# Performance work log

Measured on AMD Instinct MI355X. Metric: run time of the kernel, lower is better.

Reference implementation:

```python
import jax, jax.numpy as jnp
import numpy as np

EPS = 1e-5

def _ln(x, g, b):
    m = jnp.mean(x, axis=-1, keepdims=True)
    v = jnp.mean((x - m) ** 2, axis=-1, keepdims=True)
    return (x - m) * jax.lax.rsqrt(v + EPS) * g + b

def setup_inputs() -> dict:
    key = jax.random.key(0)
    B, T, V, D = 32, 512, 16, 128
    ks = jax.random.split(key, 22)
    rn = lambda k, shp, sc: jax.random.normal(k, shp, jnp.float32) * sc
    inp = {
        "x": rn(ks[0], (B, T, V), 1.0),
        # per-variable GRN params (stacked over the V variables)
        "W1": rn(ks[1], (V, D), 1.0),          # fc1: Linear(1, D) weight per var
        "b1": rn(ks[2], (V, D), 0.02),
        "W2": rn(ks[3], (V, D, D), 1.0 / np.sqrt(D)),   # fc2: Linear(D, D)
        "b2": rn(ks[4], (V, D), 0.02),
        "Wg": rn(ks[5], (V, D, D), 1.0 / np.sqrt(D)),   # gate: Linear(D, D)
        "bg": rn(ks[6], (V, D), 0.02),
        "Ws": rn(ks[7], (V, D), 1.0),          # skip: Linear(1, D)
        "bs": rn(ks[8], (V, D), 0.02),
        "gamma": jnp.ones((V, D), jnp.float32),
        "beta": jnp.zeros((V, D), jnp.float32),
        # softmax GRN params: d_in = V*D, d_hidden = D, d_out = V
        "sW1": rn(ks[9], (D, V * D), 1.0 / np.sqrt(V * D)),
        "sb1": rn(ks[10], (D,), 0.02),
        "sW2": rn(ks[11], (V, D), 1.0 / np.sqrt(D)),
        "sb2": rn(ks[12], (V,), 0.02),
        "sWg": rn(ks[13], (V, D), 1.0 / np.sqrt(D)),
        "sbg": rn(ks[14], (V,), 0.02),
        "sWs": rn(ks[15], (V, V * D), 1.0 / np.sqrt(V * D)),
        "sbs": rn(ks[16], (V,), 0.02),
        "sgamma": jnp.ones((V,), jnp.float32),
        "sbeta": jnp.zeros((V,), jnp.float32),
    }
    return inp

def reference(x, W1, b1, W2, b2, Wg, bg, Ws, bs, gamma, beta,
              sW1, sb1, sW2, sb2, sWg, sbg, sWs, sbs, sgamma, sbeta):
    V, D = W1.shape
    lead = x.shape[:-1]
    xf = x.reshape(-1, V)                                  # (N, V)
    # ---- all per-variable GRNs batched over the var dim ----
    h = jax.nn.elu(xf[..., None] * W1 + b1)                # (N, V, D)
    h2 = jnp.einsum('nvd,vod->nvo', h, W2) + b2            # (N, V, D)
    g = jax.nn.sigmoid(jnp.einsum('nvd,vod->nvo', h, Wg) + bg)
    skip = xf[..., None] * Ws + bs                         # (N, V, D)
    stacked = _ln(g * h2 + (1.0 - g) * skip, gamma, beta)  # (N, V, D)
    # ---- softmax GRN over flattened embeddings ----
    flat = stacked.reshape(-1, V * D)                      # (N, V*D)
    hs = jax.nn.elu(flat @ sW1.T + sb1)                    # (N, D)
    h2s = hs @ sW2.T + sb2                                 # (N, V)
    gs = jax.nn.sigmoid(hs @ sWg.T + sbg)
    sks = flat @ sWs.T + sbs
    weights = jax.nn.softmax(_ln(gs * h2s + (1.0 - gs) * sks, sgamma, sbeta), axis=-1)
    processed = jnp.einsum('nvd,nv->nd', stacked, weights) # (N, D)
    return processed.reshape(*lead, D), weights.reshape(*lead, V)
```

## Files before the change

kernel.cpp:

```cpp
#include <hip/hip_runtime.h>
#include <hip/hip_bf16.h>
#include <math.h>

#define NVAR 16
#define ND 128
#define NVD 2048
#define NROWS 16384
#define RTA 256
#define NRB 32

typedef short s16x8 __attribute__((ext_vector_type(8)));
typedef short s16x4 __attribute__((ext_vector_type(4)));
typedef float f32x4 __attribute__((ext_vector_type(4)));
typedef unsigned short u16;

#define MFMA(a,b,c) __builtin_amdgcn_mfma_f32_16x16x32_bf16((a),(b),(c),0,0,0)

#define OFF_W2  0
#define OFF_WG  262144
#define OFF_SW1 524288
#define OFF_SWS 786432
#define OFF_SW2 819200
#define OFF_SWG 821248
#define WS_ELEMS 823296
#define OFF_STK 823296
#define STK_ELEMS ((size_t)NROWS*NVD)
#define WS_NEEDED_BYTES (((size_t)WS_ELEMS + STK_ELEMS)*2)
#define SV_ELEMS ((size_t)(NROWS/16)*2048)

__device__ __forceinline__ unsigned f2bf(float f){
    union { float f; unsigned u; } c; c.f = f;
    unsigned u = c.u;
    u += 0x7fffu + ((u >> 16) & 1u);
    return u >> 16;
}
__device__ __forceinline__ float bf2f(unsigned bits){
    union { unsigned u; float f; } c; c.u = bits << 16;
    return c.f;
}
__device__ __forceinline__ float eluf(float x){ return x > 0.f ? x : __expf(x) - 1.f; }
__device__ __forceinline__ float sigm(float x){
    return __builtin_amdgcn_rcpf(1.f + __expf(-x));
}

__device__ __forceinline__ int offHs(int r, int c){
    return r*128 + ((((c>>3) ^ (r&7))<<3) | (c&7));
}
__device__ __forceinline__ int offBig(int r, int c){
    return r*2048 + ((((c>>3) ^ (r&7))<<3) | (c&7));
}

__global__ void prep_kernel(const float* __restrict__ W2, const float* __restrict__ Wg,
                            const float* __restrict__ sW1, const float* __restrict__ sWs,
                            const float* __restrict__ sW2, const float* __restrict__ sWg,
                            u16* __restrict__ ws){
    int i = blockIdx.x*256 + threadIdx.x;
    if (i >= WS_ELEMS) return;
    float v;
    if      (i < OFF_WG)  v = W2[i];
    else if (i < OFF_SW1) v = Wg[i-OFF_WG];
    else if (i < OFF_SWS) v = sW1[i-OFF_SW1];
    else if (i < OFF_SW2) v = sWs[i-OFF_SWS];
    else if (i < OFF_SWG) v = sW2[i-OFF_SW2];
    else                  v = sWg[i-OFF_SWG];
    ws[i] = (u16)f2bf(v);
}

__global__ __launch_bounds__(512, 2)
void vsn_varA(const float* __restrict__ x,
              const float* __restrict__ W1, const float* __restrict__ b1,
              const float* __restrict__ b2, const float* __restrict__ bg,
              const float* __restrict__ Wsk, const float* __restrict__ bsk,
              const float* __restrict__ gamma, const float* __restrict__ beta,
              u16* __restrict__ ws)
{
    __shared__ u16 lw2[128*128];
    __shared__ u16 lwg[128*128];
    __shared__ float lp[8*128];
    __shared__ float lxv[RTA];

    const int t = threadIdx.x, w = t>>6, l = t&63;
    const int hr = l>>4, c16 = l&15;
    const int v = blockIdx.y;
    const int row0 = blockIdx.x*RTA;

    #pragma unroll
    for (int i=0;i<8;++i){
        int cid = i*512 + t;
        int mat = cid>>11, within = cid&2047;
        int r = within>>4, c8 = within&15;
        const u16* src = ws + (mat? OFF_WG:OFF_W2) + v*16384 + r*128 + c8*8;
        s16x8 val = *reinterpret_cast<const s16x8*>(src);
        u16* dst = (mat? lwg:lw2) + r*128 + ((c8 ^ (r&7))<<3);
        *reinterpret_cast<s16x8*>(dst) = val;
    }
    if (t < 128){
        lp[t]     = W1[v*ND+t];    lp[128+t] = b1[v*ND+t];
        lp[256+t] = b2[v*ND+t];    lp[384+t] = bg[v*ND+t];
        lp[512+t] = Wsk[v*ND+t];   lp[640+t] = bsk[v*ND+t];
        lp[768+t] = gamma[v*ND+t]; lp[896+t] = beta[v*ND+t];
    }
    if (t < RTA) lxv[t] = x[(size_t)(row0+t)*NVAR + v];
    __syncthreads();

    #pragma unroll 1
    for (int pass=0; pass<2; ++pass){
        const int lrow0 = (w + pass*8)*16;
        const float xv = lxv[lrow0 + c16];

        s16x8 B[4];
        #pragma unroll
        for (int ks=0;ks<4;++ks){
            s16x8 o;
            #pragma unroll
            for (int j=0;j<8;++j){
                int c = ks*32 + hr*8 + j;
                o[j] = (short)f2bf(eluf(xv*lp[c] + lp[128+c]));
            }
            B[ks] = o;
        }
        __builtin_amdgcn_sched_barrier(0);

        float y[8][4];
        #pragma unroll
        for (int ct=0; ct<8; ++ct){
            f32x4 a2 = {0.f,0.f,0.f,0.f}, ag = {0.f,0.f,0.f,0.f};
            const int wr = ct*16 + c16;
            #pragma unroll
            for (int ks=0;ks<4;++ks){
                int chunk = (ks*4 + hr) ^ (wr&7);
                s16x8 A2 = *reinterpret_cast<const s16x8*>(lw2 + wr*128 + chunk*8);
                a2 = MFMA(A2, B[ks], a2);
            }
            #pragma unroll
            for (int ks=0;ks<4;++ks){
                int chunk = (ks*4 + hr) ^ (wr&7);
                s16x8 Ag = *reinterpret_cast<const s16x8*>(lwg + wr*128 + chunk*8);
                ag = MFMA(Ag, B[ks], ag);
            }
            const int obb = ct*16 + hr*4;
            float4 b2v = *reinterpret_cast<const float4*>(&lp[256+obb]);
            float4 bgv = *reinterpret_cast<const float4*>(&lp[384+obb]);
            float4 wsv = *reinterpret_cast<const float4*>(&lp[512+obb]);
            float4 bsv = *reinterpret_cast<const float4*>(&lp[640+obb]);
            #pragma unroll
            for (int j=0;j<4;++j){
                float h2 = a2[j] + reinterpret_cast<const float*>(&b2v)[j];
                float gg = sigm(ag[j] + reinterpret_cast<const float*>(&bgv)[j]);
                float sk = xv*reinterpret_cast<const float*>(&wsv)[j]
                           + reinterpret_cast<const float*>(&bsv)[j];
                y[ct][j] = gg*h2 + (1.f-gg)*sk;
            }
            __builtin_amdgcn_sched_barrier(0);
        }
        float s = 0.f, q = 0.f;
        #pragma unroll
        for (int ct=0;ct<8;++ct)
            #pragma unroll
            for (int j=0;j<4;++j){ float yy = y[ct][j]; s += yy; q += yy*yy; }
        s += __shfl_xor(s, 16); s += __shfl_xor(s, 32);
        q += __shfl_xor(q, 16); q += __shfl_xor(q, 32);
        float mean = s*(1.f/ND);
        float inv  = rsqrtf(q*(1.f/ND) - mean*mean + 1e-5f);

        const int grp = blockIdx.x*16 + w + pass*8;
        u16* stkb = ws + OFF_STK + (size_t)v*SV_ELEMS + (size_t)grp*2048;
        #pragma unroll
        for (int ctp=0; ctp<4; ++ctp){
            s16x4 o0, o1;
            {
                int ct = ctp*2;
                const int obb = ct*16 + hr*4;
                float4 gm = *reinterpret_cast<const float4*>(&lp[768+obb]);
                float4 bt = *reinterpret_cast<const float4*>(&lp[896+obb]);
                #pragma unroll
                for (int j=0;j<4;++j){
                    float z = (y[ct][j]-mean)*inv*reinterpret_cast<const float*>(&gm)[j]
                              + reinterpret_cast<const float*>(&bt)[j];
                    o0[j] = (short)f2bf(z);
                }
            }
            {
                int ct = ctp*2 + 1;
                const int obb = ct*16 + hr*4;
                float4 gm = *reinterpret_cast<const float4*>(&lp[768+obb]);
                float4 bt = *reinterpret_cast<const float4*>(&lp[896+obb]);
                #pragma unroll
                for (int j=0;j<4;++j){
                    float z = (y[ct][j]-mean)*inv*reinterpret_cast<const float*>(&gm)[j]
                              + reinterpret_cast<const float*>(&bt)[j];
                    o1[j] = (short)f2bf(z);
                }
            }
            u16* bp = stkb + ctp*512 + c16*32;
            *reinterpret_cast<s16x4*>(bp + hr*4)      = o0;
            *reinterpret_cast<s16x4*>(bp + 16 + hr*4) = o1;
            __builtin_amdgcn_sched_barrier(0);
        }
    }
}

__device__ __forceinline__ s16x8 ldA(const u16* abuf, int vrel, int rg, int ctp, int n, int hr){
    int base = (((vrel*2 + rg)*4 + ctp)*16 + n)*32;
    int fn = (n>>1)&3;
    return *reinterpret_cast<const s16x8*>(abuf + base + ((hr ^ fn)<<3));
}

__global__ __launch_bounds__(256, 4)
void vsn_softB(const u16* __restrict__ ws,
               const float* __restrict__ sb1, const float* __restrict__ sb2,
               const float* __restrict__ sbg, const float* __restrict__ sbs,
               const float* __restrict__ sgamma, const float* __restrict__ sbeta,
               float* __restrict__ out_proc, float* __restrict__ out_w)
{
    __shared__ u16   abuf[8192];
    __shared__ u16   hsb[32*128];
    __shared__ float pps_[2*32*16];
    __shared__ float pph[32*16];
    __shared__ float ppg[32*16];
    __shared__ float sksf[32*16];
    __shared__ float wgtb[32*16];

    float* pps = pps_;

    const int t = threadIdx.x, w = t>>6, l = t&63;
    const int hr = l>>4, c16 = l&15;
    const int row0 = blockIdx.x * NRB;
    const int grp0 = row0 >> 4;
    const int col0 = w*32;
    const int rgs = w & 1;
    const int khf = w >> 1;

    const u16* stk  = ws + OFF_STK;
    const u16* sW1b = ws + OFF_SW1;
    const u16* sWsb = ws + OFF_SWS;

    f32x4 accHs00 = {0,0,0,0}, accHs01 = {0,0,0,0};
    f32x4 accHs10 = {0,0,0,0}, accHs11 = {0,0,0,0};
    f32x4 accSk = {0,0,0,0};

    #pragma unroll 1
    for (int kt=0; kt<8; ++kt){
        #pragma unroll
        for (int i=0;i<4;++i){
            int cid = i*256 + t;
            int vv  = kt*2 + (cid>>9);
            int n   = (cid>>2)&15;
            int u   = cid&3;
            const u16* src = stk + (size_t)vv*SV_ELEMS + (size_t)(grp0+((cid>>8)&1))*2048
                           + ((cid>>2)&63)*32 + u*8;
            s16x8 val = *reinterpret_cast<const s16x8*>(src);
            *reinterpret_cast<s16x8*>(abuf + (cid>>2)*32 + ((u ^ ((n>>1)&3))<<3)) = val;
        }
        __syncthreads();
        #pragma unroll
        for (int ks=0; ks<8; ++ks){
            const u16* bbase = sW1b + (size_t)(col0 + c16)*NVD + kt*256 + ks*32 + hr*8;
            s16x8 bf0 = *reinterpret_cast<const s16x8*>(bbase);
            s16x8 bf1 = *reinterpret_cast<const s16x8*>(bbase + (size_t)16*NVD);
            s16x8 af0 = ldA(abuf, ks>>2, 0, ks&3, c16, hr);
            s16x8 af1 = ldA(abuf, ks>>2, 1, ks&3, c16, hr);
            accHs00 = MFMA(af0, bf0, accHs00);
            accHs10 = MFMA(af1, bf0, accHs10);
            accHs01 = MFMA(af0, bf1, accHs01);
            accHs11 = MFMA(af1, bf1, accHs11);
        }
        #pragma unroll
        for (int kk=0; kk<4; ++kk){
            int ks = khf*4 + kk;
            s16x8 bf = *reinterpret_cast<const s16x8*>(
                sWsb + (size_t)c16*NVD + kt*256 + ks*32 + hr*8);
            s16x8 af = ldA(abuf, ks>>2, rgs, ks&3, c16, hr);
            accSk = MFMA(af, bf, accSk);
        }
        __syncthreads();
    }

    {
        float bb0 = sb1[col0 + c16];
        float bb1 = sb1[col0 + 16 + c16];
        #pragma unroll
        for (int j=0;j<4;++j){
            int r0 = hr*4 + j, r1 = 16 + hr*4 + j;
            hsb[offHs(r0, col0 + c16)]      = (u16)f2bf(eluf(accHs00[j] + bb0));
            hsb[offHs(r1, col0 + c16)]      = (u16)f2bf(eluf(accHs10[j] + bb0));
            hsb[offHs(r0, col0 + 16 + c16)] = (u16)f2bf(eluf(accHs01[j] + bb1));
            hsb[offHs(r1, col0 + 16 + c16)] = (u16)f2bf(eluf(accHs11[j] + bb1));
        }
        #pragma unroll
        for (int j=0;j<4;++j)
            pps[khf*512 + (rgs*16 + hr*4 + j)*16 + c16] = accSk[j];
    }
    __syncthreads();

    #pragma unroll
    for (int i=0;i<2;++i){
        int idx = i*256 + t;
        sksf[idx] = pps[idx] + pps[512+idx] + sbs[idx&15];
    }
    {
        const u16* Bsrc = (w < 2) ? (ws + OFF_SW2) : (ws + OFF_SWG);
        int rg = w & 1;
        f32x4 acc = {0,0,0,0};
        #pragma unroll
        for (int ks=0; ks<4; ++ks){
            int rr = rg*16 + c16;
            int chunk = (ks*4 + hr) ^ (rr&7);
            s16x8 af = *reinterpret_cast<const s16x8*>(hsb + rr*128 + chunk*8);
            s16x8 bf = *reinterpret_cast<const s16x8*>(Bsrc + c16*ND + ks*32 + hr*8);
            acc = MFMA(af, bf, acc);
        }
        float* dst = (w < 2) ? pph : ppg;
        #pragma unroll
        for (int j=0;j<4;++j)
            dst[(rg*16 + hr*4 + j)*16 + c16] = acc[j];
    }
    __syncthreads();

    #pragma unroll
    for (int it=0; it<2; ++it){
        int r = it*16 + (t>>4), vv = t & 15;
        float h2s = pph[r*16+vv] + sb2[vv];
        float gs  = sigm(ppg[r*16+vv] + sbg[vv]);
        float yv  = gs*h2s + (1.f-gs)*sksf[r*16+vv];
        float ssum = yv, qsum = yv*yv;
        #pragma unroll
        for (int m=1;m<16;m<<=1){ ssum += __shfl_xor(ssum,m,16); qsum += __shfl_xor(qsum,m,16); }
        float mean = ssum*(1.f/NVAR);
        float var  = qsum*(1.f/NVAR) - mean*mean;
        float z = (yv-mean)*rsqrtf(var+1e-5f)*sgamma[vv] + sbeta[vv];
        float mx = z;
        #pragma unroll
        for (int m=1;m<16;m<<=1) mx = fmaxf(mx, __shfl_xor(mx,m,16));
        float e = __expf(z-mx);
        float es = e;
        #pragma unroll
        for (int m=1;m<16;m<<=1) es += __shfl_xor(es,m,16);
        float wgt = e * __builtin_amdgcn_rcpf(es);
        wgtb[r*16+vv] = wgt;
        out_w[(size_t)(row0+r)*NVAR + vv] = wgt;
    }
    __syncthreads();

    #pragma unroll
    for (int it=0; it<2; ++it){
        int idx = it*256 + t;
        int r = idx>>4, cu = idx&15;
        int ctp = cu>>2, u = cu&3;
        int grp = (row0+r)>>4, n = r&15;
        float acc[8] = {0,0,0,0,0,0,0,0};
        #pragma unroll
        for (int v=0; v<NVAR; ++v){
            float wv = wgtb[r*16 + v];
            const u16* sp = stk + (size_t)v*SV_ELEMS + (size_t)grp*2048
                          + (ctp*16+n)*32 + u*8;
            s16x8 sv = *reinterpret_cast<const s16x8*>(sp);
            #pragma unroll
            for (int k=0;k<8;++k) acc[k] += bf2f((u16)sv[k]) * wv;
        }
        float* op = out_proc + (size_t)(row0+r)*ND + ctp*32 + u*8;
        float4 lo = { acc[0], acc[1], acc[2], acc[3] };
        float4 hi = { acc[4], acc[5], acc[6], acc[7] };
        *reinterpret_cast<float4*>(op)     = lo;
        *reinterpret_cast<float4*>(op + 4) = hi;
    }
}

__global__ __launch_bounds__(512, 4)
void vsn_fused(const float* __restrict__ x,
               const float* __restrict__ W1, const float* __restrict__ b1,
               const float* __restrict__ b2, const float* __restrict__ bg,
               const float* __restrict__ Wsk, const float* __restrict__ bsk,
               const float* __restrict__ gamma, const float* __restrict__ beta,
               const float* __restrict__ sb1, const float* __restrict__ sb2,
               const float* __restrict__ sbg, const float* __restrict__ sbs,
               const float* __restrict__ sgamma, const float* __restrict__ sbeta,
               const u16* __restrict__ ws,
               float* __restrict__ out_proc, float* __restrict__ out_w)
{
    __shared__ u16   big[16*2048];
    __shared__ u16   hsb[16*128];
    __shared__ float pp[8*256];
    __shared__ float psumbuf[256];
    __shared__ float sksbuf[256];
    __shared__ float sx[256];

    float* psum  = psumbuf;
    float* psum2 = psumbuf + 128;

    const int t   = threadIdx.x;
    const int w   = t >> 6;
    const int l   = t & 63;
    const int hr  = l >> 4;
    const int c16 = l & 15;
    const int row0 = blockIdx.x * 16;
    const int orow = w*16 + c16;

    if (t < 256) sx[t] = x[row0*NVAR + t];
    __syncthreads();

    const u16* W2b = ws + OFF_W2;
    const u16* Wgb = ws + OFF_WG;

    for (int v = 0; v < NVAR; ++v){
        #pragma unroll
        for (int i = 0; i < 4; ++i){
            int idx = i*512 + t;
            int r = idx >> 7, d = idx & 127;
            float hv = eluf(sx[r*NVAR+v]*W1[v*ND+d] + b1[v*ND+d]);
            big[offBig(r, v*ND+d)] = (u16)f2bf(hv);
        }
        __syncthreads();

        s16x8 A[4];
        #pragma unroll
        for (int ks = 0; ks < 4; ++ks)
            A[ks] = *reinterpret_cast<const s16x8*>(&big[offBig(c16, v*ND + ks*32 + hr*8)]);
        const s16x8* B2p = reinterpret_cast<const s16x8*>(W2b + v*ND*ND + orow*ND + hr*8);
        const s16x8* Bgp = reinterpret_cast<const s16x8*>(Wgb + v*ND*ND + orow*ND + hr*8);
        f32x4 acc2 = {0.f,0.f,0.f,0.f}, accg = {0.f,0.f,0.f,0.f};
        #pragma unroll
        for (int ks = 0; ks < 4; ++ks) acc2 = MFMA(A[ks], B2p[ks*4], acc2);
        #pragma unroll
        for (int ks = 0; ks < 4; ++ks) accg = MFMA(A[ks], Bgp[ks*4], accg);

        const float b2v = b2[v*ND+orow], bgv = bg[v*ND+orow];
        const float wsv = Wsk[v*ND+orow], bsv = bsk[v*ND+orow];
        float y[4];
        #pragma unroll
        for (int j = 0; j < 4; ++j){
            int r = hr*4 + j;
            float h2 = acc2[j] + b2v;
            float g  = sigm(accg[j] + bgv);
            float sk = sx[r*NVAR+v]*wsv + bsv;
            y[j] = g*h2 + (1.f-g)*sk;
        }
        float s[4], q[4];
        #pragma unroll
        for (int j=0;j<4;++j){ s[j]=y[j]; q[j]=y[j]*y[j]; }
        #pragma unroll
        for (int m=1; m<16; m<<=1){
            #pragma unroll
            for (int j=0;j<4;++j){
                s[j] += __shfl_xor(s[j], m, 16);
                q[j] += __shfl_xor(q[j], m, 16);
            }
        }
        if (c16 == 0){
            #pragma unroll
            for (int j=0;j<4;++j){
                psum [(hr*4+j)*8 + w] = s[j];
                psum2[(hr*4+j)*8 + w] = q[j];
            }
        }
        __syncthreads();

        if (t < 16){
            float ss=0.f, qq=0.f;
            #pragma unroll
            for (int ww=0; ww<8; ++ww){ ss += psum[t*8+ww]; qq += psum2[t*8+ww]; }
            float mean = ss*(1.f/ND);
            float var  = qq*(1.f/ND) - mean*mean;
            sksbuf[t]      = mean;
            sksbuf[16 + t] = rsqrtf(var + 1e-5f);
        }
        __syncthreads();

        const float gm = gamma[v*ND+orow], bt = beta[v*ND+orow];
        #pragma unroll
        for (int j=0;j<4;++j){
            int r = hr*4 + j;
            float z = (y[j]-sksbuf[r])*sksbuf[16+r]*gm + bt;
            big[offBig(r, v*ND+orow)] = (u16)f2bf(z);
        }
    }
    __syncthreads();

    const u16* sW1b = ws + OFF_SW1;
    {
        f32x4 acc0 = {0,0,0,0}, acc1 = {0,0,0,0};
        const s16x8* Bp = reinterpret_cast<const s16x8*>(sW1b + orow*NVD + hr*8);
        #pragma unroll 8
        for (int ks = 0; ks < 64; ks += 2){
            s16x8 A0 = *reinterpret_cast<const s16x8*>(&big[offBig(c16, ks*32 + hr*8)]);
            s16x8 A1 = *reinterpret_cast<const s16x8*>(&big[offBig(c16, (ks+1)*32 + hr*8)]);
            acc0 = MFMA(A0, Bp[ks*4],     acc0);
            acc1 = MFMA(A1, Bp[(ks+1)*4], acc1);
        }
        float bb = sb1[orow];
        #pragma unroll
        for (int j=0;j<4;++j){
            int r = hr*4 + j;
            hsb[offHs(r, orow)] = (u16)f2bf(eluf(acc0[j] + acc1[j] + bb));
        }
    }
    const u16* sWsb = ws + OFF_SWS;
    {
        f32x4 acc = {0,0,0,0};
        const s16x8* Bp = reinterpret_cast<const s16x8*>(sWsb + c16*NVD + hr*8);
        #pragma unroll
        for (int kk = 0; kk < 8; ++kk){
            int ks = w*8 + kk;
            s16x8 Af = *reinterpret_cast<const s16x8*>(&big[offBig(c16, ks*32 + hr*8)]);
            acc = MFMA(Af, Bp[ks*4], acc);
        }
        #pragma unroll
        for (int j=0;j<4;++j)
            pp[w*256 + (hr*4+j)*16 + c16] = acc[j];
    }
    __syncthreads();

    if (t < 256){
        float a = sbs[t & 15];
        #pragma unroll
        for (int ww=0; ww<8; ++ww) a += pp[ww*256 + t];
        sksbuf[t] = a;
    }
    __syncthreads();

    {
        const u16* Bsrc = (w < 4) ? (ws + OFF_SW2) : (ws + OFF_SWG);
        const int m = w & 3;
        s16x8 Af = *reinterpret_cast<const s16x8*>(&hsb[offHs(c16, m*32 + hr*8)]);
        s16x8 Bf = *reinterpret_cast<const s16x8*>(Bsrc + c16*ND + m*32 + hr*8);
        f32x4 z4 = {0,0,0,0};
        f32x4 acc = MFMA(Af, Bf, z4);
        #pragma unroll
        for (int j=0;j<4;++j)
            pp[w*256 + (hr*4+j)*16 + c16] = acc[j];
    }
    __syncthreads();

    if (t < 256){
        int r = t >> 4, vv = t & 15;
        float h2s = sb2[vv], gp = sbg[vv];
        #pragma unroll
        for (int j=0;j<4;++j){ h2s += pp[j*256 + t]; gp += pp[(4+j)*256 + t]; }
        float gs = sigm(gp);
        float yv = gs*h2s + (1.f-gs)*sksbuf[t];
        float ssum = yv, qsum = yv*yv;
        #pragma unroll
        for (int m=1;m<16;m<<=1){ ssum += __shfl_xor(ssum,m,16); qsum += __shfl_xor(qsum,m,16); }
        float mean = ssum*(1.f/NVAR);
        float var  = qsum*(1.f/NVAR) - mean*mean;
        float z = (yv-mean)*rsqrtf(var+1e-5f)*sgamma[vv] + sbeta[vv];
        float mx = z;
        #pragma unroll
        for (int m=1;m<16;m<<=1) mx = fmaxf(mx, __shfl_xor(mx,m,16));
        float e = __expf(z-mx);
        float es = e;
        #pragma unroll
        for (int m=1;m<16;m<<=1) es += __shfl_xor(es,m,16);
        float wgt = e/es;
        psumbuf[t] = wgt;
        out_w[(row0+r)*NVAR + vv] = wgt;
    }
    __syncthreads();

    if (t < 256){
        int r = t >> 4, d8 = (t & 15)*8;
        float acc[8] = {0,0,0,0,0,0,0,0};
        #pragma unroll
        for (int v=0; v<NVAR; ++v){
            float wv = psumbuf[r*NVAR + v];
            s16x8 sv = *reinterpret_cast<const s16x8*>(&big[offBig(r, v*ND + d8)]);
            #pragma unroll
            for (int k=0;k<8;++k) acc[k] += bf2f((u16)sv[k]) * wv;
        }
        float* op = &out_proc[(row0+r)*ND + d8];
        #pragma unroll
        for (int k=0;k<8;++k) op[k] = acc[k];
    }
}

extern "C" void kernel_launch(void* const* d_in, const int* in_sizes, int n_in,
                              void* d_out, int out_size, void* d_ws, size_t ws_size,
                              hipStream_t stream) {
    (void)in_sizes; (void)n_in; (void)out_size;
    const float* x     = (const float*)d_in[0];
    const float* W1    = (const float*)d_in[1];
    const float* b1    = (const float*)d_in[2];
    const float* W2    = (const float*)d_in[3];
    const float* b2    = (const float*)d_in[4];
    const float* Wg    = (const float*)d_in[5];
    const float* bg    = (const float*)d_in[6];
    const float* Wsk   = (const float*)d_in[7];
    const float* bsk   = (const float*)d_in[8];
    const float* gamma = (const float*)d_in[9];
    const float* beta  = (const float*)d_in[10];
    const float* sW1   = (const float*)d_in[11];
    const float* sb1   = (const float*)d_in[12];
    const float* sW2   = (const float*)d_in[13];
    const float* sb2   = (const float*)d_in[14];
    const float* sWg   = (const float*)d_in[15];
    const float* sbg   = (const float*)d_in[16];
    const float* sWs   = (const float*)d_in[17];
    const float* sbs   = (const float*)d_in[18];
    const float* sgam  = (const float*)d_in[19];
    const float* sbet  = (const float*)d_in[20];

    u16* ws = (u16*)d_ws;
    float* out_proc = (float*)d_out;
    float* out_w    = out_proc + (size_t)NROWS * ND;

    prep_kernel<<<(WS_ELEMS + 255)/256, 256, 0, stream>>>(W2, Wg, sW1, sWs, sW2, sWg, ws);

    if (ws_size >= WS_NEEDED_BYTES) {
        vsn_varA<<<dim3(NROWS/RTA, NVAR), 512, 0, stream>>>(
            x, W1, b1, b2, bg, Wsk, bsk, gamma, beta, ws);
        vsn_softB<<<NROWS/NRB, 256, 0, stream>>>(
            ws, sb1, sb2, sbg, sbs, sgam, sbet, out_proc, out_w);
    } else {
        vsn_fused<<<NROWS/16, 512, 0, stream>>>(
            x, W1, b1, b2, bg, Wsk, bsk, gamma, beta,
            sb1, sb2, sbg, sbs, sgam, sbet, ws, out_proc, out_w);
    }
}
```

Before: 113.1 us.

## Double-buffer stacked-activation tiles in softmax GRN kernel with register prefetch

Converts the K-loop of the softmax-GRN kernel to a double-buffered LDS scheme. The next tile's stacked activations are loaded into registers before the MFMA work on the current tile and written to the alternate buffer afterwards, so one barrier per iteration is removed and global latency is hidden behind compute. The cost is 16 KB more shared memory per block, which may reduce occupancy under launch_bounds(256,4), plus extra live registers for the prefetched tiles.

```diff
diff --git a/kernel.cpp b/kernel.cpp
--- a/kernel.cpp
+++ b/kernel.cpp
@@ -213,7 +213,7 @@
                const float* __restrict__ sgamma, const float* __restrict__ sbeta,
                float* __restrict__ out_proc, float* __restrict__ out_w)
 {
-    __shared__ u16   abuf[8192];
+    __shared__ u16   abuf[2*8192];
     __shared__ u16   hsb[32*128];
     __shared__ float pps_[2*32*16];
     __shared__ float pph[32*16];
@@ -235,31 +235,48 @@
     const u16* sW1b = ws + OFF_SW1;
     const u16* sWsb = ws + OFF_SWS;
 
+    const int c0 = t, c1 = 256+t, c2 = 512+t, c3 = 768+t;
+    #define SRCOFF(cid) ((size_t)(grp0+(((cid)>>8)&1))*2048 + (size_t)(((cid)>>2)&63)*32 + ((cid)&3)*8)
+    #define VREL(cid)   ((cid)>>9)
+    #define DSTOFF(cid) (((cid)>>2)*32 + ((((cid)&3) ^ ((((cid)>>3)&3)))<<3))
+    const size_t s0 = SRCOFF(c0), s1 = SRCOFF(c1), s2 = SRCOFF(c2), s3 = SRCOFF(c3);
+    const int    v0 = VREL(c0),   v1 = VREL(c1),   v2 = VREL(c2),   v3 = VREL(c3);
+    const int    d0 = DSTOFF(c0), d1 = DSTOFF(c1), d2 = DSTOFF(c2), d3 = DSTOFF(c3);
+
     f32x4 accHs00 = {0,0,0,0}, accHs01 = {0,0,0,0};
     f32x4 accHs10 = {0,0,0,0}, accHs11 = {0,0,0,0};
     f32x4 accSk = {0,0,0,0};
 
+    s16x8 t0 = *reinterpret_cast<const s16x8*>(stk + (size_t)(0+v0)*SV_ELEMS + s0);
+    s16x8 t1 = *reinterpret_cast<const s16x8*>(stk + (size_t)(0+v1)*SV_ELEMS + s1);
+    s16x8 t2 = *reinterpret_cast<const s16x8*>(stk + (size_t)(0+v2)*SV_ELEMS + s2);
+    s16x8 t3 = *reinterpret_cast<const s16x8*>(stk + (size_t)(0+v3)*SV_ELEMS + s3);
+    *reinterpret_cast<s16x8*>(abuf + d0) = t0;
+    *reinterpret_cast<s16x8*>(abuf + d1) = t1;
+    *reinterpret_cast<s16x8*>(abuf + d2) = t2;
+    *reinterpret_cast<s16x8*>(abuf + d3) = t3;
+    int cur = 0;
+
     #pragma unroll 1
     for (int kt=0; kt<8; ++kt){
-        #pragma unroll
-        for (int i=0;i<4;++i){
-            int cid = i*256 + t;
-            int vv  = kt*2 + (cid>>9);
-            int n   = (cid>>2)&15;
-            int u   = cid&3;
-            const u16* src = stk + (size_t)vv*SV_ELEMS + (size_t)(grp0+((cid>>8)&1))*2048
-                           + ((cid>>2)&63)*32 + u*8;
-            s16x8 val = *reinterpret_cast<const s16x8*>(src);
-            *reinterpret_cast<s16x8*>(abuf + (cid>>2)*32 + ((u ^ ((n>>1)&3))<<3)) = val;
-        }
+        if (kt < 7){
+            int vvb = (kt+1)*2;
+            t0 = *reinterpret_cast<const s16x8*>(stk + (size_t)(vvb+v0)*SV_ELEMS + s0);
+            t1 = *reinterpret_cast<const s16x8*>(stk + (size_t)(vvb+v1)*SV_ELEMS + s1);
+            t2 = *reinterpret_cast<const s16x8*>(stk + (size_t)(vvb+v2)*SV_ELEMS + s2);
+            t3 = *reinterpret_cast<const s16x8*>(stk + (size_t)(vvb+v3)*SV_ELEMS + s3);
+        }
+        __builtin_amdgcn_sched_barrier(0);
         __syncthreads();
+        const u16* abr = abuf + cur*8192;
+
         #pragma unroll
         for (int ks=0; ks<8; ++ks){
             const u16* bbase = sW1b + (size_t)(col0 + c16)*NVD + kt*256 + ks*32 + hr*8;
             s16x8 bf0 = *reinterpret_cast<const s16x8*>(bbase);
             s16x8 bf1 = *reinterpret_cast<const s16x8*>(bbase + (size_t)16*NVD);
-            s16x8 af0 = ldA(abuf, ks>>2, 0, ks&3, c16, hr);
-            s16x8 af1 = ldA(abuf, ks>>2, 1, ks&3, c16, hr);
+            s16x8 af0 = ldA(abr, ks>>2, 0, ks&3, c16, hr);
+            s16x8 af1 = ldA(abr, ks>>2, 1, ks&3, c16, hr);
             accHs00 = MFMA(af0, bf0, accHs00);
             accHs10 = MFMA(af1, bf0, accHs10);
             accHs01 = MFMA(af0, bf1, accHs01);
@@ -270,11 +287,20 @@
             int ks = khf*4 + kk;
             s16x8 bf = *reinterpret_cast<const s16x8*>(
                 sWsb + (size_t)c16*NVD + kt*256 + ks*32 + hr*8);
-            s16x8 af = ldA(abuf, ks>>2, rgs, ks&3, c16, hr);
+            s16x8 af = ldA(abr, ks>>2, rgs, ks&3, c16, hr);
             accSk = MFMA(af, bf, accSk);
         }
-        __syncthreads();
-    }
+
+        if (kt < 7){
+            u16* abw = abuf + (cur^1)*8192;
+            *reinterpret_cast<s16x8*>(abw + d0) = t0;
+            *reinterpret_cast<s16x8*>(abw + d1) = t1;
+            *reinterpret_cast<s16x8*>(abw + d2) = t2;
+            *reinterpret_cast<s16x8*>(abw + d3) = t3;
+        }
+        cur ^= 1;
+    }
+    __syncthreads();
 
     {
         float bb0 = sb1[col0 + c16];
```

Measured after the change: 110.8 us. -2.1%, faster.
